# Performance work log

Hardware: AMD Instinct MI355X
Metric: run time of the kernel (lower is better)

The kernel has to match this reference:

```python
import jax, jax.numpy as jnp
import numpy as np


def setup_inputs() -> dict:
    key = jax.random.key(0)
    k1, k2, k3 = jax.random.split(key, 3)
    B, T, IN, OUT, S = 256, 512, 256, 256, 128
    x = jax.random.normal(k1, (B, T, IN), dtype=jnp.float32)
    subject_id = jax.random.randint(k2, (B,), 0, S, dtype=jnp.int64)
    weights = jax.random.normal(k3, (S, IN, OUT), dtype=jnp.float32) * 0.01
    biases = jnp.zeros((S, 1, OUT), dtype=jnp.float32)
    return {"x": x, "subject_id": subject_id, "weights": weights, "biases": biases}


def reference(x, subject_id, weights, biases):
    # Gather per-subject weight [B, in, out] and bias [B, 1, out], then batched matmul.
    w = weights[subject_id]            # [B, in, out]
    b = biases[subject_id]             # [B, 1, out]
    return jnp.einsum("bti,bio->bto", x, w) + b
```

## Files before the change

### kernel.cpp

```cpp
#include <hip/hip_runtime.h>
#include <hip/hip_bf16.h>


#define B_DIM 256
#define T_DIM 512
#define IN_DIM 256
#define OUT_DIM 256
#define S_DIM 128

typedef __attribute__((ext_vector_type(4))) float f32x4;
typedef __attribute__((ext_vector_type(8))) short s16x8;
typedef __attribute__((ext_vector_type(8))) unsigned short u16x8;
typedef __attribute__((ext_vector_type(4))) unsigned short u16x4;

static __device__ __forceinline__ unsigned short f2bf(float f) {
  __hip_bfloat16 h = __float2bfloat16(f);
  return __builtin_bit_cast(unsigned short, h);
}

__global__ __launch_bounds__(256) void wt_transpose(const float* __restrict__ w,
                                                    unsigned short* __restrict__ wT2) {
  __shared__ float tile[64][65];
  int bid = blockIdx.x;
  int s = bid >> 4, ti = (bid >> 2) & 3, to = bid & 3;
  const float* wp = w + (size_t)s * IN_DIM * OUT_DIM;
  int t = threadIdx.x;
  int rr = t >> 6, cc = t & 63;
#pragma unroll
  for (int p = 0; p < 16; ++p) {
    tile[p * 4 + rr][cc] = wp[(size_t)(ti * 64 + p * 4 + rr) * OUT_DIM + to * 64 + cc];
  }
  __syncthreads();
  int orr = t >> 4, i4 = (t & 15) * 4;
#pragma unroll
  for (int p = 0; p < 4; ++p) {
    int ol = p * 16 + orr;
    int i0 = ti * 64 + i4;
    u16x4 v;
    v[0] = f2bf(tile[i4 + 0][ol]);
    v[1] = f2bf(tile[i4 + 1][ol]);
    v[2] = f2bf(tile[i4 + 2][ol]);
    v[3] = f2bf(tile[i4 + 3][ol]);
    size_t idx = ((size_t)(s * 32 + (i0 >> 3)) * OUT_DIM + (to * 64 + ol)) * 8 + (i0 & 7);
    *(u16x4*)(wT2 + idx) = v;
  }
}

__global__ __launch_bounds__(512) void subj_gemm_v13(
    const float* __restrict__ x, const int* __restrict__ sid,
    const unsigned short* __restrict__ wT2, const float* __restrict__ bias,
    float* __restrict__ out) {
  __shared__ __align__(16) unsigned short lA[128 * IN_DIM];

  unsigned wg = blockIdx.x;
  unsigned bid = (wg & 7u) * 128u + (wg >> 3);
  int batch = bid >> 2;
  int mt = bid & 3;
  int s = sid[batch];

  int t = threadIdx.x;
  int l = t & 63, wv = t >> 6;
  int wn = wv * 32;
  int fr = l & 15, kq = l >> 4;
  int r0 = kq * 4;

  const float* xbase = x + ((size_t)batch * T_DIM + mt * 128) * IN_DIM;
  const unsigned short* wbase = wT2 + (size_t)s * 32 * OUT_DIM * 8;

#define LOADB(dst, stp)                                                       \
  do {                                                                        \
    _Pragma("unroll") for (int fn = 0; fn < 2; ++fn)                          \
        dst[fn] = *(const s16x8*)(wbase +                                     \
                                  ((size_t)((stp) * 4 + kq) * OUT_DIM + wn +  \
                                   fn * 16 + fr) * 8);                        \
  } while (0)

  s16x8 bA[2], bB[2];
  LOADB(bA, 0);

  {
    f32x4 aR[4][4];
#pragma unroll
    for (int j = 0; j < 4; ++j)
#pragma unroll
      for (int p = 0; p < 4; ++p)
        aR[j][p] = *(const f32x4*)(xbase + (size_t)j * 8192 + t * 16 + p * 4);
#pragma unroll
    for (int j = 0; j < 4; ++j)
#pragma unroll
      for (int h = 0; h < 2; ++h) {
        int cf = j * 1024 + 2 * t + h;
        int row = cf >> 5, c = cf & 31;
        u16x8 v;
        v[0] = f2bf(aR[j][2 * h][0]); v[1] = f2bf(aR[j][2 * h][1]);
        v[2] = f2bf(aR[j][2 * h][2]); v[3] = f2bf(aR[j][2 * h][3]);
        v[4] = f2bf(aR[j][2 * h + 1][0]); v[5] = f2bf(aR[j][2 * h + 1][1]);
        v[6] = f2bf(aR[j][2 * h + 1][2]); v[7] = f2bf(aR[j][2 * h + 1][3]);
        *(u16x8*)((unsigned char*)&lA[0] + row * 512 + ((c ^ (row & 15)) << 4)) = v;
      }
  }
  __syncthreads();

  f32x4 acc[8][2];
#pragma unroll
  for (int i = 0; i < 8; ++i)
#pragma unroll
    for (int j = 0; j < 2; ++j) acc[i][j] = (f32x4){0.f, 0.f, 0.f, 0.f};

#define AFRAG(dst, stp)                                                       \
  do {                                                                        \
    _Pragma("unroll") for (int fm = 0; fm < 8; ++fm) {                        \
      int row = fm * 16 + fr;                                                 \
      unsigned c = (unsigned)((stp) * 4 + kq);                                \
      dst[fm] = *(const s16x8*)((const unsigned char*)&lA[0] + row * 512 +    \
                                ((c ^ (unsigned)(row & 15)) << 4));           \
    }                                                                         \
  } while (0)
#define MFMA_STEP(breg)                                                       \
  do {                                                                        \
    _Pragma("unroll") for (int fm = 0; fm < 8; ++fm)                          \
      _Pragma("unroll") for (int fn = 0; fn < 2; ++fn)                        \
          acc[fm][fn] = __builtin_amdgcn_mfma_f32_16x16x32_bf16(              \
              af[fm], breg[fn], acc[fm][fn], 0, 0, 0);                        \
  } while (0)

  s16x8 af[8];
#pragma unroll
  for (int sp = 0; sp < 8; sp += 2) {
    LOADB(bB, sp + 1);
    AFRAG(af, sp);
    MFMA_STEP(bA);
    if (sp + 2 < 8) LOADB(bA, sp + 2);
    AFRAG(af, sp + 1);
    MFMA_STEP(bB);
  }

  const float* bp = bias + (size_t)s * OUT_DIM + wn;
  float bv[2];
#pragma unroll
  for (int fn = 0; fn < 2; ++fn) bv[fn] = bp[fn * 16 + fr];

  float* orow = out + ((size_t)batch * T_DIM + mt * 128) * OUT_DIM + wn;
#pragma unroll
  for (int fm = 0; fm < 8; ++fm)
#pragma unroll
    for (int r = 0; r < 4; ++r)
#pragma unroll
      for (int fn = 0; fn < 2; ++fn)
        orow[(size_t)(fm * 16 + r0 + r) * OUT_DIM + fn * 16 + fr] =
            acc[fm][fn][r] + bv[fn];
#undef LOADB
#undef AFRAG
#undef MFMA_STEP
}

__global__ __launch_bounds__(256) void naive_kernel(
    const float* __restrict__ x, const int* __restrict__ sid,
    const float* __restrict__ w, const float* __restrict__ bias,
    float* __restrict__ out) {
  __shared__ float lx[IN_DIM];
  size_t bt = blockIdx.x;
  int batch = (int)(bt / T_DIM);
  int s = sid[batch];
  int o = threadIdx.x;
  lx[o] = x[bt * IN_DIM + o];
  __syncthreads();
  const float* wp = w + (size_t)s * IN_DIM * OUT_DIM + o;
  float acc = bias[(size_t)s * OUT_DIM + o];
  for (int i = 0; i < IN_DIM; ++i) acc += lx[i] * wp[(size_t)i * OUT_DIM];
  out[bt * OUT_DIM + o] = acc;
}

extern "C" void kernel_launch(void* const* d_in, const int* in_sizes, int n_in,
                              void* d_out, int out_size, void* d_ws, size_t ws_size,
                              hipStream_t stream) {
  const float* x = (const float*)d_in[0];
  const int* sid = (const int*)d_in[1];
  const float* w = (const float*)d_in[2];
  const float* bias = (const float*)d_in[3];
  float* out = (float*)d_out;

  size_t need = (size_t)S_DIM * IN_DIM * OUT_DIM * sizeof(unsigned short);
  if (ws_size >= need) {
    unsigned short* wT2 = (unsigned short*)d_ws;
    wt_transpose<<<dim3(S_DIM * 16), dim3(256), 0, stream>>>(w, wT2);
    subj_gemm_v13<<<dim3(1024), dim3(512), 0, stream>>>(x, sid, wT2, bias, out);
  } else {
    naive_kernel<<<dim3(B_DIM * T_DIM), dim3(256), 0, stream>>>(x, sid, w, bias, out);
  }
}
```

Baseline: 83.39 us.

## Make GEMM persistent per batch with register-prefetched x tiles and resident weights

Each workgroup now handles a whole batch (four 128-row tiles) instead of one tile. The subject's weight fragments are loaded into registers once, and the next x tile's global loads are issued while the current tile is converted and multiplied. This cuts redundant weight loads and overlaps x fetch with compute. In exchange the grid shrinks from 1024 to 256 workgroups, so there may be fewer waves in flight than compute units can hold, and register pressure rises.

```diff
diff --git a/kernel.cpp b/kernel.cpp
--- a/kernel.cpp
+++ b/kernel.cpp
@@ -46,16 +46,14 @@
   }
 }
 
-__global__ __launch_bounds__(512) void subj_gemm_v13(
+__global__ __launch_bounds__(512) void subj_gemm_v14(
     const float* __restrict__ x, const int* __restrict__ sid,
     const unsigned short* __restrict__ wT2, const float* __restrict__ bias,
     float* __restrict__ out) {
   __shared__ __align__(16) unsigned short lA[128 * IN_DIM];
 
   unsigned wg = blockIdx.x;
-  unsigned bid = (wg & 7u) * 128u + (wg >> 3);
-  int batch = bid >> 2;
-  int mt = bid & 3;
+  int batch = (int)((wg & 7u) * 32u + (wg >> 3));
   int s = sid[batch];
 
   int t = threadIdx.x;
@@ -64,94 +62,100 @@
   int fr = l & 15, kq = l >> 4;
   int r0 = kq * 4;
 
-  const float* xbase = x + ((size_t)batch * T_DIM + mt * 128) * IN_DIM;
+  const float* xb = x + (size_t)batch * T_DIM * IN_DIM;
   const unsigned short* wbase = wT2 + (size_t)s * 32 * OUT_DIM * 8;
 
-#define LOADB(dst, stp)                                                       \
-  do {                                                                        \
-    _Pragma("unroll") for (int fn = 0; fn < 2; ++fn)                          \
-        dst[fn] = *(const s16x8*)(wbase +                                     \
-                                  ((size_t)((stp) * 4 + kq) * OUT_DIM + wn +  \
-                                   fn * 16 + fr) * 8);                        \
-  } while (0)
-
-  s16x8 bA[2], bB[2];
-  LOADB(bA, 0);
-
-  {
-    f32x4 aR[4][4];
+  s16x8 breg[2][8];
 #pragma unroll
-    for (int j = 0; j < 4; ++j)
+  for (int stp = 0; stp < 8; ++stp)
 #pragma unroll
-      for (int p = 0; p < 4; ++p)
-        aR[j][p] = *(const f32x4*)(xbase + (size_t)j * 8192 + t * 16 + p * 4);
-#pragma unroll
-    for (int j = 0; j < 4; ++j)
-#pragma unroll
-      for (int h = 0; h < 2; ++h) {
-        int cf = j * 1024 + 2 * t + h;
-        int row = cf >> 5, c = cf & 31;
-        u16x8 v;
-        v[0] = f2bf(aR[j][2 * h][0]); v[1] = f2bf(aR[j][2 * h][1]);
-        v[2] = f2bf(aR[j][2 * h][2]); v[3] = f2bf(aR[j][2 * h][3]);
-        v[4] = f2bf(aR[j][2 * h + 1][0]); v[5] = f2bf(aR[j][2 * h + 1][1]);
-        v[6] = f2bf(aR[j][2 * h + 1][2]); v[7] = f2bf(aR[j][2 * h + 1][3]);
-        *(u16x8*)((unsigned char*)&lA[0] + row * 512 + ((c ^ (row & 15)) << 4)) = v;
-      }
-  }
-  __syncthreads();
-
-  f32x4 acc[8][2];
-#pragma unroll
-  for (int i = 0; i < 8; ++i)
-#pragma unroll
-    for (int j = 0; j < 2; ++j) acc[i][j] = (f32x4){0.f, 0.f, 0.f, 0.f};
-
-#define AFRAG(dst, stp)                                                       \
-  do {                                                                        \
-    _Pragma("unroll") for (int fm = 0; fm < 8; ++fm) {                        \
-      int row = fm * 16 + fr;                                                 \
-      unsigned c = (unsigned)((stp) * 4 + kq);                                \
-      dst[fm] = *(const s16x8*)((const unsigned char*)&lA[0] + row * 512 +    \
-                                ((c ^ (unsigned)(row & 15)) << 4));           \
-    }                                                                         \
-  } while (0)
-#define MFMA_STEP(breg)                                                       \
-  do {                                                                        \
-    _Pragma("unroll") for (int fm = 0; fm < 8; ++fm)                          \
-      _Pragma("unroll") for (int fn = 0; fn < 2; ++fn)                        \
-          acc[fm][fn] = __builtin_amdgcn_mfma_f32_16x16x32_bf16(              \
-              af[fm], breg[fn], acc[fm][fn], 0, 0, 0);                        \
-  } while (0)
-
-  s16x8 af[8];
-#pragma unroll
-  for (int sp = 0; sp < 8; sp += 2) {
-    LOADB(bB, sp + 1);
-    AFRAG(af, sp);
-    MFMA_STEP(bA);
-    if (sp + 2 < 8) LOADB(bA, sp + 2);
-    AFRAG(af, sp + 1);
-    MFMA_STEP(bB);
-  }
+    for (int fn = 0; fn < 2; ++fn)
+      breg[fn][stp] = *(const s16x8*)(wbase +
+                                      ((size_t)(stp * 4 + kq) * OUT_DIM + wn +
+                                       fn * 16 + fr) * 8);
 
   const float* bp = bias + (size_t)s * OUT_DIM + wn;
   float bv[2];
 #pragma unroll
   for (int fn = 0; fn < 2; ++fn) bv[fn] = bp[fn * 16 + fr];
 
-  float* orow = out + ((size_t)batch * T_DIM + mt * 128) * OUT_DIM + wn;
+  f32x4 aR[16];
+#define ISSUE_A(at)                                                           \
+  do {                                                                        \
+    const float* xt = xb + (size_t)(at) * 128 * IN_DIM;                       \
+    _Pragma("unroll") for (int j = 0; j < 4; ++j)                             \
+      _Pragma("unroll") for (int p = 0; p < 4; ++p)                           \
+        aR[j * 4 + p] = *(const f32x4*)(xt + (size_t)j * 8192 + t * 16 + p * 4); \
+  } while (0)
+#define CVT_WRITE()                                                           \
+  do {                                                                        \
+    _Pragma("unroll") for (int j = 0; j < 4; ++j)                             \
+      _Pragma("unroll") for (int h = 0; h < 2; ++h) {                         \
+        int cf = j * 1024 + 2 * t + h;                                        \
+        int row = cf >> 5, c = cf & 31;                                       \
+        u16x8 v;                                                              \
+        v[0] = f2bf(aR[j * 4 + 2 * h][0]); v[1] = f2bf(aR[j * 4 + 2 * h][1]); \
+        v[2] = f2bf(aR[j * 4 + 2 * h][2]); v[3] = f2bf(aR[j * 4 + 2 * h][3]); \
+        v[4] = f2bf(aR[j * 4 + 2 * h + 1][0]);                                \
+        v[5] = f2bf(aR[j * 4 + 2 * h + 1][1]);                                \
+        v[6] = f2bf(aR[j * 4 + 2 * h + 1][2]);                                \
+        v[7] = f2bf(aR[j * 4 + 2 * h + 1][3]);                                \
+        *(u16x8*)((unsigned char*)&lA[0] + row * 512 +                        \
+                  ((c ^ (row & 15)) << 4)) = v;                               \
+      }                                                                       \
+  } while (0)
+
+  ISSUE_A(0);
+
 #pragma unroll
-  for (int fm = 0; fm < 8; ++fm)
+  for (int at = 0; at < 4; ++at) {
+    if (at == 0) asm volatile("s_waitcnt vmcnt(0)");
+    else         asm volatile("s_waitcnt vmcnt(63)");
+    __builtin_amdgcn_sched_barrier(0);
+    CVT_WRITE();
+    if (at < 3) ISSUE_A(at + 1);
+    asm volatile("s_waitcnt lgkmcnt(0)");
+    __builtin_amdgcn_sched_barrier(0);
+    __syncthreads();
+
+    f32x4 acc[8][2];
 #pragma unroll
-    for (int r = 0; r < 4; ++r)
+    for (int i = 0; i < 8; ++i)
 #pragma unroll
-      for (int fn = 0; fn < 2; ++fn)
-        orow[(size_t)(fm * 16 + r0 + r) * OUT_DIM + fn * 16 + fr] =
-            acc[fm][fn][r] + bv[fn];
-#undef LOADB
-#undef AFRAG
-#undef MFMA_STEP
+      for (int j = 0; j < 2; ++j) acc[i][j] = (f32x4){0.f, 0.f, 0.f, 0.f};
+
+#pragma unroll
+    for (int stp = 0; stp < 8; ++stp) {
+      s16x8 af[8];
+#pragma unroll
+      for (int fm = 0; fm < 8; ++fm) {
+        int row = fm * 16 + fr;
+        unsigned c = (unsigned)(stp * 4) + (unsigned)kq;
+        af[fm] = *(const s16x8*)((const unsigned char*)&lA[0] + row * 512 +
+                                 ((c ^ (unsigned)(row & 15)) << 4));
+      }
+#pragma unroll
+      for (int fm = 0; fm < 8; ++fm)
+#pragma unroll
+        for (int fn = 0; fn < 2; ++fn)
+          acc[fm][fn] = __builtin_amdgcn_mfma_f32_16x16x32_bf16(
+              af[fm], breg[fn][stp], acc[fm][fn], 0, 0, 0);
+    }
+
+    __syncthreads();
+
+    float* orow = out + ((size_t)batch * T_DIM + at * 128) * OUT_DIM + wn;
+#pragma unroll
+    for (int fm = 0; fm < 8; ++fm)
+#pragma unroll
+      for (int r = 0; r < 4; ++r)
+#pragma unroll
+        for (int fn = 0; fn < 2; ++fn)
+          orow[(size_t)(fm * 16 + r0 + r) * OUT_DIM + fn * 16 + fr] =
+              acc[fm][fn][r] + bv[fn];
+  }
+#undef ISSUE_A
+#undef CVT_WRITE
 }
 
 __global__ __launch_bounds__(256) void naive_kernel(
@@ -184,7 +188,7 @@
   if (ws_size >= need) {
     unsigned short* wT2 = (unsigned short*)d_ws;
     wt_transpose<<<dim3(S_DIM * 16), dim3(256), 0, stream>>>(w, wT2);
-    subj_gemm_v13<<<dim3(1024), dim3(512), 0, stream>>>(x, sid, wT2, bias, out);
+    subj_gemm_v14<<<dim3(256), dim3(512), 0, stream>>>(x, sid, wT2, bias, out);
   } else {
     naive_kernel<<<dim3(B_DIM * T_DIM), dim3(256), 0, stream>>>(x, sid, w, bias, out);
   }
```

Measured after the change: 128.7 us. 1.54x slower.
